# Optimization experiments

Measured on AMD Instinct MI355X. Metric: run time of the kernel, lower is better.

Reference implementation:

```python
import jax, jax.numpy as jnp
import numpy as np

N, E = 50000, 1600000
DIM_IN, HEADS, DIM_OUT = 256, 4, 32
NEG_SLOPE = 0.2


def setup_inputs() -> dict:
    key = jax.random.key(0)
    k1, k2, k3, k4, k5, k6 = jax.random.split(key, 6)
    x = jax.random.normal(k1, (N, DIM_IN), dtype=jnp.float32)
    edge_index = jax.random.randint(k2, (2, E), 0, N, dtype=jnp.int64)
    s = 1.0 / np.sqrt(DIM_IN)
    W = jax.random.normal(k3, (DIM_IN, HEADS * DIM_OUT), dtype=jnp.float32) * s
    att_src = jax.random.normal(k4, (HEADS, DIM_OUT), dtype=jnp.float32) * 0.1
    att_dst = jax.random.normal(k5, (HEADS, DIM_OUT), dtype=jnp.float32) * 0.1
    bias = jax.random.normal(k6, (HEADS * DIM_OUT,), dtype=jnp.float32) * 0.01
    return {"x": x, "edge_index": edge_index, "W": W,
            "att_src": att_src, "att_dst": att_dst, "bias": bias}


def reference(x, edge_index, W, att_src, att_dst, bias):
    n = x.shape[0]
    h, c = att_src.shape
    # linear projection, per-head view [N, H, C]
    xp = (x @ W).reshape(n, h, c)
    # per-node attention logits [N, H]
    a_src = jnp.einsum('nhc,hc->nh', xp, att_src)
    a_dst = jnp.einsum('nhc,hc->nh', xp, att_dst)
    # add self loops (PyG default add_self_loops=True)
    loops = jnp.arange(n, dtype=edge_index.dtype)
    src = jnp.concatenate([edge_index[0], loops])  # [E+N]
    dst = jnp.concatenate([edge_index[1], loops])
    # edge attention scores [E+N, H]
    e = jax.nn.leaky_relu(a_src[src] + a_dst[dst], negative_slope=NEG_SLOPE)
    # segment softmax over incoming edges of each dst node
    emax = jax.ops.segment_max(e, dst, num_segments=n)
    ex = jnp.exp(e - emax[dst])
    denom = jax.ops.segment_sum(ex, dst, num_segments=n)
    alpha = ex / denom[dst]  # [E+N, H]
    # weighted scatter-aggregate of src features
    msg = xp[src] * alpha[:, :, None]  # [E+N, H, C]
    out = jax.ops.segment_sum(msg, dst, num_segments=n)  # [N, H, C]
    return out.reshape(n, h * c) + bias
```

## Files before the change

kernel.cpp:

```cpp
#include <hip/hip_runtime.h>
#include <hip/hip_fp16.h>


#define DIN 256
#define HC 128
#define NH 4
#define NEG 0.2f
#define BCAP 12288
#define LOG2E 1.44269504f

typedef _Float16 half8 __attribute__((ext_vector_type(8)));
typedef _Float16 half2v __attribute__((ext_vector_type(2)));
typedef float f32x4 __attribute__((ext_vector_type(4)));

__device__ __forceinline__ void proj_body(char* sm, int tid, const float* __restrict__ x,
                                          const _Float16* __restrict__ Wt,
                                          const float* __restrict__ attS,
                                          const float* __restrict__ attD,
                                          __half* __restrict__ xph,
                                          float* __restrict__ a_src,
                                          float* __restrict__ a_dst, int n, int node0) {
    _Float16* xs = (_Float16*)sm;
    _Float16* Wl = (_Float16*)(sm + 5120);
    _Float16* ep = (_Float16*)sm;
    float* attSL = (float*)(sm + 17408);
    float* attDL = (float*)(sm + 17920);

    const int wave = tid >> 6;
    const int lane = tid & 63;
    const int l15  = lane & 15;
    const int quad = lane >> 4;

    if (tid < 128) attSL[tid] = attS[tid];
    else           attDL[tid - 128] = attD[tid - 128];

    f32x4 acc[8];
#pragma unroll
    for (int ct = 0; ct < 8; ++ct) acc[ct] = (f32x4){0.f, 0.f, 0.f, 0.f};

    for (int kt = 0; kt < DIN; kt += 32) {
        __syncthreads();
#pragma unroll
        for (int r = 0; r < 4; ++r) {
            int idx = tid + r * 256;
            int row = idx >> 4;
            int kp  = idx & 15;
            int gn = node0 + row;
            float2 xv = make_float2(0.f, 0.f);
            if (gn < n) xv = *(const float2*)&x[(size_t)gn * DIN + kt + kp * 2];
            half2v p; p[0] = (_Float16)xv.x; p[1] = (_Float16)xv.y;
            *(half2v*)&xs[row * 40 + kp * 2] = p;
        }
#pragma unroll
        for (int r = 0; r < 2; ++r) {
            int id = tid + r * 256;
            int c = id >> 2;
            int q = id & 3;
            half8 wv = *(const half8*)&Wt[(size_t)c * 256 + kt + q * 8];
            *(half8*)&Wl[c * 40 + q * 8] = wv;
        }
        __syncthreads();
        half8 af = *(const half8*)&xs[(wave * 16 + l15) * 40 + quad * 8];
#pragma unroll
        for (int ct = 0; ct < 8; ++ct) {
            half8 bf = *(const half8*)&Wl[(ct * 16 + l15) * 40 + quad * 8];
            acc[ct] = __builtin_amdgcn_mfma_f32_16x16x32_f16(af, bf, acc[ct], 0, 0, 0);
        }
    }
    __syncthreads();
#pragma unroll
    for (int ct = 0; ct < 8; ++ct)
#pragma unroll
        for (int r = 0; r < 4; ++r) {
            int row = wave * 16 + quad * 4 + r;
            ep[row * 136 + ct * 16 + l15] = (_Float16)acc[ct][r];
        }
    __syncthreads();
    {
        int row = tid >> 2, ch = tid & 3;
        int node = node0 + row;
        if (node < n) {
            const uint4* s = (const uint4*)&ep[row * 136 + ch * 32];
            uint4* d = (uint4*)&xph[(size_t)node * HC + ch * 32];
            d[0] = s[0]; d[1] = s[1]; d[2] = s[2]; d[3] = s[3];
        }
    }
    {
        int nl = tid >> 2, h = tid & 3;
        int node = node0 + nl;
        if (node < n) {
            float ps = 0.f, pd = 0.f;
            const _Float16* er = &ep[nl * 136 + h * 32];
#pragma unroll
            for (int c = 0; c < 32; ++c) {
                float v = (float)er[c];
                ps += v * attSL[h * 32 + c];
                pd += v * attDL[h * 32 + c];
            }
            a_src[node * NH + h] = ps * LOG2E;
            a_dst[node * NH + h] = pd * LOG2E;
        }
    }
}

__global__ __launch_bounds__(256) void k_zero_wtrans(int* __restrict__ gz,
                                                     const float* __restrict__ W,
                                                     _Float16* __restrict__ Wt) {
    const int b = blockIdx.x;
    if (b < 2) {
        gz[b * 256 + threadIdx.x] = 0;
    } else {
        int i = (b - 2) * 256 + threadIdx.x;
        int k = i >> 7, c = i & 127;
        Wt[c * 256 + k] = (_Float16)W[i];
    }
}

__global__ __launch_bounds__(512) void k_bin_proj(const int* __restrict__ ei,
                                                  int* __restrict__ gcur0,
                                                  unsigned* __restrict__ binned,
                                                  const float* __restrict__ x,
                                                  const _Float16* __restrict__ Wt,
                                                  const float* __restrict__ attS,
                                                  const float* __restrict__ attD,
                                                  __half* __restrict__ xph,
                                                  float* __restrict__ a_src,
                                                  float* __restrict__ a_dst,
                                                  int e, int n, int ech) {
    __shared__ __attribute__((aligned(16))) char sm[36864];
    if ((int)blockIdx.x < ech) {
        int* h     = (int*)sm;
        int* rbase = (int*)(sm + 1024);
        const int tid = threadIdx.x;
        if (tid < 256) h[tid] = 0;
        __syncthreads();
        const int base = blockIdx.x * 4096;
        unsigned pk[8];
        int bk[8];
#pragma unroll
        for (int j = 0; j < 8; ++j) {
            int i = base + j * 512 + tid;
            bk[j] = -1;
            if (i < e) {
                int src = ei[i];
                int dst = ei[e + i];
                if ((unsigned)dst < (unsigned)n && (unsigned)src < (unsigned)n) {
                    bk[j] = dst >> 8;
                    pk[j] = ((unsigned)(dst & 255) << 16) | (unsigned)src;
                    atomicAdd(&h[bk[j]], 1);
                }
            }
        }
        __syncthreads();
        if (tid < 256) {
            if (h[tid]) rbase[tid] = atomicAdd(&gcur0[tid], h[tid]);
            h[tid] = 0;
        }
        __syncthreads();
#pragma unroll
        for (int j = 0; j < 8; ++j) {
            if (bk[j] >= 0) {
                int p = atomicAdd(&h[bk[j]], 1);
                int pib = rbase[bk[j]] + p;
                if (pib < BCAP) binned[(size_t)bk[j] * BCAP + pib] = pk[j];
            }
        }
    } else {
        const int sub = threadIdx.x >> 8;
        const int tid = threadIdx.x & 255;
        const int tile = ((int)blockIdx.x - ech) * 2 + sub;
        proj_body(sm + sub * 18432, tid, x, Wt, attS, attD, xph, a_src, a_dst, n, tile * 64);
    }
}

__global__ __launch_bounds__(1024) void k_csr(const unsigned* __restrict__ binned,
                                              const int* __restrict__ gcnt,
                                              int* __restrict__ off,
                                              int* __restrict__ deg,
                                              unsigned short* __restrict__ srt,
                                              int n) {
    __shared__ int cnt[256], buf[256], cur[256];
    const int tid = threadIdx.x;
    const int b = blockIdx.x;
    if (tid < 256) { buf[tid] = min(gcnt[tid], BCAP); cnt[tid] = 0; }
    __syncthreads();
    for (int s = 1; s < 256; s <<= 1) {
        int t = (tid < 256 && tid >= s) ? buf[tid - s] : 0;
        __syncthreads();
        if (tid < 256) buf[tid] += t;
        __syncthreads();
    }
    const int cb = min(gcnt[b], BCAP);
    const int excl = buf[b] - cb;
    const int pgbase = ((excl + 31) & ~31) + b * 8192;
    const int kb = b * BCAP;
    const int ke = kb + cb;
    __syncthreads();
    for (int i = kb + tid; i < ke; i += 1024)
        atomicAdd(&cnt[binned[i] >> 16], 1);
    __syncthreads();
    int v = 0;
    if (tid < 256) { v = cnt[tid]; buf[tid] = (v + 31) & ~31; }
    __syncthreads();
    for (int s = 1; s < 256; s <<= 1) {
        int t = (tid < 256 && tid >= s) ? buf[tid - s] : 0;
        __syncthreads();
        if (tid < 256) buf[tid] += t;
        __syncthreads();
    }
    if (tid < 256) {
        const int myoff = pgbase + buf[tid] - ((v + 31) & ~31);
        const int node = b * 256 + tid;
        if (node < n) { off[node] = myoff; deg[node] = v; }
        cur[tid] = myoff;
    }
    __syncthreads();
    for (int i = kb + tid; i < ke; i += 1024) {
        unsigned pv = binned[i];
        int nl = pv >> 16;
        int pos = atomicAdd(&cur[nl], 1);
        srt[pos] = (unsigned short)(pv & 0xFFFFu);
    }
}

__global__ __launch_bounds__(256) void agg_kernel(const __half* __restrict__ xph,
                                                  const float* __restrict__ a_src,
                                                  const float* __restrict__ a_dst,
                                                  const int* __restrict__ off,
                                                  const int* __restrict__ deg,
                                                  const unsigned short* __restrict__ srt,
                                                  const float* __restrict__ bias,
                                                  float* __restrict__ out, int n) {
    const int node = (blockIdx.x * blockDim.x + threadIdx.x) >> 6;
    if (node >= n) return;
    const int lane = threadIdx.x & 63;
    const int g = lane >> 4;
    const unsigned l = (unsigned)(lane & 15);
    const unsigned h = l >> 2;
    const unsigned lo8 = l * 8u;

    const float ad = a_dst[((unsigned)node << 2) + h];

    float acc[8];
#pragma unroll
    for (int c = 0; c < 8; ++c) acc[c] = 0.f;
    float den = 0.f;

    if (g == 0) {
        float t = a_src[((unsigned)node << 2) + h] + ad;
        float s = exp2f(fmaxf(t, NEG * t));
        half8 xv = *(const half8*)&xph[((unsigned)node << 7) + lo8];
#pragma unroll
        for (int c = 0; c < 8; ++c) acc[c] = s * (float)xv[c];
        den = s;
    }

    const int kb = off[node];
    const int ke = kb + deg[node];
    int k0 = kb;
    for (; k0 + 16 <= ke; k0 += 16) {
        const unsigned kg = (unsigned)(k0 + g * 4);
        const ushort4 s4 = *(const ushort4*)&srt[kg];
        unsigned sv[4] = {s4.x, s4.y, s4.z, s4.w};
        float asv[4];
        half8 hv[4];
#pragma unroll
        for (int j = 0; j < 4; ++j) asv[j] = a_src[(sv[j] << 2) + h];
#pragma unroll
        for (int j = 0; j < 4; ++j)
            hv[j] = *(const half8*)&xph[(sv[j] << 7) + lo8];
#pragma unroll
        for (int j = 0; j < 4; ++j) {
            float t = asv[j] + ad;
            const float s = exp2f(fmaxf(t, NEG * t));
#pragma unroll
            for (int c = 0; c < 8; ++c) acc[c] += s * (float)hv[j][c];
            den += s;
        }
    }
    if (k0 < ke) {
        const unsigned kg = (unsigned)(k0 + g * 4);
        const ushort4 s4 = *(const ushort4*)&srt[kg];
        const unsigned sv[4] = {s4.x, s4.y, s4.z, s4.w};
#pragma unroll
        for (int j = 0; j < 4; ++j) {
            if ((int)kg + j < ke) {
                float t = a_src[(sv[j] << 2) + h] + ad;
                const float s = exp2f(fmaxf(t, NEG * t));
                const half8 hv = *(const half8*)&xph[(sv[j] << 7) + lo8];
#pragma unroll
                for (int c = 0; c < 8; ++c) acc[c] += s * (float)hv[c];
                den += s;
            }
        }
    }

#pragma unroll
    for (int c = 0; c < 8; ++c) acc[c] += __shfl_xor(acc[c], 16, 64);
    den += __shfl_xor(den, 16, 64);
#pragma unroll
    for (int c = 0; c < 8; ++c) acc[c] += __shfl_xor(acc[c], 32, 64);
    den += __shfl_xor(den, 32, 64);

    if (lane < 16) {
        const float inv = 1.0f / den;
        const float4* b4 = (const float4*)&bias[lo8];
        float4 o0, o1;
        o0.x = acc[0] * inv + b4[0].x;
        o0.y = acc[1] * inv + b4[0].y;
        o0.z = acc[2] * inv + b4[0].z;
        o0.w = acc[3] * inv + b4[0].w;
        o1.x = acc[4] * inv + b4[1].x;
        o1.y = acc[5] * inv + b4[1].y;
        o1.z = acc[6] * inv + b4[1].z;
        o1.w = acc[7] * inv + b4[1].w;
        float4* d = (float4*)&out[((unsigned)node << 7) + lo8];
        d[0] = o0;
        d[1] = o1;
    }
}

extern "C" void kernel_launch(void* const* d_in, const int* in_sizes, int n_in,
                              void* d_out, int out_size, void* d_ws, size_t ws_size,
                              hipStream_t stream) {
    if (n_in < 6 || !d_out || !d_ws) return;
    const float* x    = (const float*)d_in[0];
    const int*   ei   = (const int*)d_in[1];
    const float* W    = (const float*)d_in[2];
    const float* attS = (const float*)d_in[3];
    const float* attD = (const float*)d_in[4];
    const float* bias = (const float*)d_in[5];
    float* out = (float*)d_out;

    const int N = in_sizes[0] / DIN;
    const int E = in_sizes[1] / 2;
    if (N <= 0 || E <= 0) return;
    const int NBUCK = (N + 255) >> 8;
    if (NBUCK > 256 || N > 65536) return;

    char* ws = (char*)d_ws;
    size_t off_b = 0;
    auto carve = [&](size_t bytes) {
        size_t p = off_b;
        off_b = (off_b + bytes + 255) & ~(size_t)255;
        return (void*)(ws + p);
    };
    __half*         xph    = (__half*)carve((size_t)N * HC * 2);
    _Float16*       Wt     = (_Float16*)carve((size_t)HC * DIN * 2);
    float*          a_src  = (float*)carve((size_t)N * NH * 4);
    float*          a_dst  = (float*)carve((size_t)N * NH * 4);
    int*            gz     = (int*)carve(512 * 4);
    unsigned*       binned = (unsigned*)carve((size_t)NBUCK * BCAP * 4);
    int*            offp   = (int*)carve((size_t)N * 4);
    int*            degp   = (int*)carve((size_t)N * 4);
    unsigned short* srt    = (unsigned short*)carve(((size_t)E + (size_t)NBUCK * 8192 + 64) * 2);
    (void)out_size;
    if (off_b > ws_size) return;

    int* gcur0 = gz;

    const int ECH = (E + 4095) / 4096;
    const int PB  = (N + 63) / 64;
    const int PBH = (PB + 1) / 2;

    k_zero_wtrans<<<2 + 128, 256, 0, stream>>>(gz, W, Wt);
    k_bin_proj<<<ECH + PBH, 512, 0, stream>>>(ei, gcur0, binned, x, Wt, attS, attD,
                                              xph, a_src, a_dst, E, N, ECH);
    k_csr<<<NBUCK, 1024, 0, stream>>>(binned, gcur0, offp, degp, srt, N);
    agg_kernel<<<(N * 64 + 255) / 256, 256, 0, stream>>>(xph, a_src, a_dst,
                                                         offp, degp, srt, bias, out, N);
}
```

Measured before the change: 217.1 us.

## Drop W-transpose kernel, convert W in-tile, cache binned entries in CSR registers

```diff
diff --git a/kernel.cpp b/kernel.cpp
--- a/kernel.cpp
+++ b/kernel.cpp
@@ -14,7 +14,7 @@
 typedef float f32x4 __attribute__((ext_vector_type(4)));
 
 __device__ __forceinline__ void proj_body(char* sm, int tid, const float* __restrict__ x,
-                                          const _Float16* __restrict__ Wt,
+                                          const float* __restrict__ W,
                                           const float* __restrict__ attS,
                                           const float* __restrict__ attD,
                                           __half* __restrict__ xph,
@@ -52,12 +52,15 @@
             *(half2v*)&xs[row * 40 + kp * 2] = p;
         }
 #pragma unroll
-        for (int r = 0; r < 2; ++r) {
+        for (int r = 0; r < 4; ++r) {
             int id = tid + r * 256;
-            int c = id >> 2;
-            int q = id & 3;
-            half8 wv = *(const half8*)&Wt[(size_t)c * 256 + kt + q * 8];
-            *(half8*)&Wl[c * 40 + q * 8] = wv;
+            int kk = id >> 5;
+            int c4 = (id & 31) * 4;
+            float4 wv = *(const float4*)&W[(size_t)(kt + kk) * 128 + c4];
+            Wl[(c4 + 0) * 40 + kk] = (_Float16)wv.x;
+            Wl[(c4 + 1) * 40 + kk] = (_Float16)wv.y;
+            Wl[(c4 + 2) * 40 + kk] = (_Float16)wv.z;
+            Wl[(c4 + 3) * 40 + kk] = (_Float16)wv.w;
         }
         __syncthreads();
         half8 af = *(const half8*)&xs[(wave * 16 + l15) * 40 + quad * 8];
@@ -103,24 +106,11 @@
     }
 }
 
-__global__ __launch_bounds__(256) void k_zero_wtrans(int* __restrict__ gz,
-                                                     const float* __restrict__ W,
-                                                     _Float16* __restrict__ Wt) {
-    const int b = blockIdx.x;
-    if (b < 2) {
-        gz[b * 256 + threadIdx.x] = 0;
-    } else {
-        int i = (b - 2) * 256 + threadIdx.x;
-        int k = i >> 7, c = i & 127;
-        Wt[c * 256 + k] = (_Float16)W[i];
-    }
-}
-
 __global__ __launch_bounds__(512) void k_bin_proj(const int* __restrict__ ei,
                                                   int* __restrict__ gcur0,
                                                   unsigned* __restrict__ binned,
                                                   const float* __restrict__ x,
-                                                  const _Float16* __restrict__ Wt,
+                                                  const float* __restrict__ W,
                                                   const float* __restrict__ attS,
                                                   const float* __restrict__ attD,
                                                   __half* __restrict__ xph,
@@ -169,7 +159,7 @@
         const int sub = threadIdx.x >> 8;
         const int tid = threadIdx.x & 255;
         const int tile = ((int)blockIdx.x - ech) * 2 + sub;
-        proj_body(sm + sub * 18432, tid, x, Wt, attS, attD, xph, a_src, a_dst, n, tile * 64);
+        proj_body(sm + sub * 18432, tid, x, W, attS, attD, xph, a_src, a_dst, n, tile * 64);
     }
 }
 
@@ -196,8 +186,16 @@
     const int kb = b * BCAP;
     const int ke = kb + cb;
     __syncthreads();
-    for (int i = kb + tid; i < ke; i += 1024)
-        atomicAdd(&cnt[binned[i] >> 16], 1);
+    unsigned pk[12];
+#pragma unroll
+    for (int j = 0; j < 12; ++j) {
+        int i = kb + j * 1024 + tid;
+        pk[j] = 0xFFFFFFFFu;
+        if (i < ke) {
+            pk[j] = binned[i];
+            atomicAdd(&cnt[pk[j] >> 16], 1);
+        }
+    }
     __syncthreads();
     int v = 0;
     if (tid < 256) { v = cnt[tid]; buf[tid] = (v + 31) & ~31; }
@@ -215,11 +213,13 @@
         cur[tid] = myoff;
     }
     __syncthreads();
-    for (int i = kb + tid; i < ke; i += 1024) {
-        unsigned pv = binned[i];
-        int nl = pv >> 16;
-        int pos = atomicAdd(&cur[nl], 1);
-        srt[pos] = (unsigned short)(pv & 0xFFFFu);
+#pragma unroll
+    for (int j = 0; j < 12; ++j) {
+        if (pk[j] != 0xFFFFFFFFu) {
+            int nl = pk[j] >> 16;
+            int pos = atomicAdd(&cur[nl], 1);
+            srt[pos] = (unsigned short)(pk[j] & 0xFFFFu);
+        }
     }
 }
 
@@ -231,8 +231,9 @@
                                                   const unsigned short* __restrict__ srt,
                                                   const float* __restrict__ bias,
                                                   float* __restrict__ out, int n) {
-    const int node = (blockIdx.x * blockDim.x + threadIdx.x) >> 6;
-    if (node >= n) return;
+    int node_ = (blockIdx.x * blockDim.x + threadIdx.x) >> 6;
+    if (node_ >= n) return;
+    const int node = __builtin_amdgcn_readfirstlane(node_);
     const int lane = threadIdx.x & 63;
     const int g = lane >> 4;
     const unsigned l = (unsigned)(lane & 15);
@@ -346,7 +347,6 @@
         return (void*)(ws + p);
     };
     __half*         xph    = (__half*)carve((size_t)N * HC * 2);
-    _Float16*       Wt     = (_Float16*)carve((size_t)HC * DIN * 2);
     float*          a_src  = (float*)carve((size_t)N * NH * 4);
     float*          a_dst  = (float*)carve((size_t)N * NH * 4);
     int*            gz     = (int*)carve(512 * 4);
@@ -363,8 +363,8 @@
     const int PB  = (N + 63) / 64;
     const int PBH = (PB + 1) / 2;
 
-    k_zero_wtrans<<<2 + 128, 256, 0, stream>>>(gz, W, Wt);
-    k_bin_proj<<<ECH + PBH, 512, 0, stream>>>(ei, gcur0, binned, x, Wt, attS, attD,
+    hipMemsetAsync(gcur0, 0, 256 * sizeof(int), stream);
+    k_bin_proj<<<ECH + PBH, 512, 0, stream>>>(ei, gcur0, binned, x, W, attS, attD,
                                               xph, a_src, a_dst, E, N, ECH);
     k_csr<<<NBUCK, 1024, 0, stream>>>(binned, gcur0, offp, degp, srt, N);
     agg_kernel<<<(N * 64 + 255) / 256, 256, 0, stream>>>(xph, a_src, a_dst,
```

Result: slower. 230.0 us (+5.9%).
